# Kernel optimization log

Measured on AMD Instinct MI355X. Metric: run time of the kernel, lower is better.

Reference implementation:

```python
import jax, jax.numpy as jnp
import numpy as np
from jax import lax

T, B, E, U, V = 512, 256, 512, 1024, 50257
H1, H2, L = 512, 256, 2


def setup_inputs() -> dict:
    key = jax.random.key(0)
    ks = jax.random.split(key, 12)
    s = lambda n: 1.0 / np.sqrt(n)
    return {
        "inputs": jax.random.randint(ks[0], (T, B), 0, V, dtype=jnp.int32),
        "input_lengths": jax.random.randint(ks[1], (B,), 1, T + 1, dtype=jnp.int32),
        "embedder": jax.random.normal(ks[2], (V, E), jnp.float32),
        # GRU params (TF GRUCell layout: gates over [x, h] -> 2U; candidate over [x, r*h] -> U)
        "W_gates": jax.random.normal(ks[3], (E + U, 2 * U), jnp.float32) * s(E + U),
        "b_gates": jnp.ones((2 * U,), jnp.float32),  # TF bias init 1.0
        "W_cand": jax.random.normal(ks[4], (E + U, U), jnp.float32) * s(E + U),
        "b_cand": jnp.zeros((U,), jnp.float32),
        # MLP (fully_connected default activation = relu; final layer linear)
        "W1": jax.random.normal(ks[5], (U, H1), jnp.float32) * s(U),
        "b1": jnp.zeros((H1,), jnp.float32),
        "W2": jax.random.normal(ks[6], (H1, H2), jnp.float32) * s(H1),
        "b2": jnp.zeros((H2,), jnp.float32),
        "W3": jax.random.normal(ks[7], (H2, L), jnp.float32) * s(H2),
        "b3": jnp.zeros((L,), jnp.float32),
    }


def reference(inputs, input_lengths, embedder, W_gates, b_gates, W_cand, b_cand,
              W1, b1, W2, b2, W3, b3):
    emb = embedder[inputs]  # [T, B, E] (time-major, as in batch_embedding_lookup)
    t_idx = jnp.arange(emb.shape[0], dtype=input_lengths.dtype)

    def step(h, xt):
        x, t = xt
        xh = jnp.concatenate([x, h], axis=-1)                      # [B, E+U]
        r, z = jnp.split(jax.nn.sigmoid(xh @ W_gates + b_gates), 2, axis=-1)
        cand = jnp.tanh(jnp.concatenate([x, r * h], axis=-1) @ W_cand + b_cand)
        h_new = z * h + (1.0 - z) * cand                           # TF GRUCell update
        # dynamic_rnn sequence_length semantics: state held past end of sequence
        h_out = jnp.where((t < input_lengths)[:, None], h_new, h)
        return h_out, None

    h0 = jnp.zeros((emb.shape[1], U), emb.dtype)
    h_final, _ = lax.scan(step, h0, (emb, t_idx))                  # [B, U]

    x = jax.nn.relu(h_final @ W1 + b1)
    x = jax.nn.relu(x @ W2 + b2)
    logits = x @ W3 + b3                                           # [B, 2]
    predictions = jax.nn.softmax(logits, axis=-1)
    return logits, predictions
```

## Files before the change

kernel.cpp:

```cpp
#include <hip/hip_runtime.h>

typedef unsigned short u16;
typedef unsigned int u32;
typedef unsigned long long u64;

using bf16x8 = __attribute__((ext_vector_type(8))) __bf16;
using f32x4  = __attribute__((ext_vector_type(4))) float;

#define T_DIM 512
#define B_DIM 256
#define E_DIM 512
#define U_DIM 1024
#define K_DIM 1536
#define NG    2048
#define NWG   256

__device__ __forceinline__ u16 f2bf(float f) {
  union { float f; u32 u; } v; v.f = f;
  return (u16)((v.u + 0x7fffu + ((v.u >> 16) & 1u)) >> 16);
}

#define WAIT_VM_ALL() do { asm volatile("s_waitcnt vmcnt(0)" ::: "memory"); \
                           __builtin_amdgcn_sched_barrier(0); } while (0)

#define LD16T(dst, base, OFS) \
  asm volatile("global_load_dwordx4 %0, %1, off offset:" #OFS " sc0 sc1" \
               : "=&v"(dst) : "v"(base))

#define LOAD32T(arr, b) do { \
  const u16* _b0 = (b);           const u16* _b1 = (b) + 2048;  \
  const u16* _b2 = (b) + 4096;    const u16* _b3 = (b) + 6144;  \
  const u16* _b4 = (b) + 8192;    const u16* _b5 = (b) + 10240; \
  const u16* _b6 = (b) + 12288;   const u16* _b7 = (b) + 14336; \
  LD16T(arr[0],  _b0, 0); LD16T(arr[1],  _b0, 1024); \
  LD16T(arr[2],  _b0, 2048); LD16T(arr[3],  _b0, 3072); \
  LD16T(arr[4],  _b1, 0); LD16T(arr[5],  _b1, 1024); \
  LD16T(arr[6],  _b1, 2048); LD16T(arr[7],  _b1, 3072); \
  LD16T(arr[8],  _b2, 0); LD16T(arr[9],  _b2, 1024); \
  LD16T(arr[10], _b2, 2048); LD16T(arr[11], _b2, 3072); \
  LD16T(arr[12], _b3, 0); LD16T(arr[13], _b3, 1024); \
  LD16T(arr[14], _b3, 2048); LD16T(arr[15], _b3, 3072); \
  LD16T(arr[16], _b4, 0); LD16T(arr[17], _b4, 1024); \
  LD16T(arr[18], _b4, 2048); LD16T(arr[19], _b4, 3072); \
  LD16T(arr[20], _b5, 0); LD16T(arr[21], _b5, 1024); \
  LD16T(arr[22], _b5, 2048); LD16T(arr[23], _b5, 3072); \
  LD16T(arr[24], _b6, 0); LD16T(arr[25], _b6, 1024); \
  LD16T(arr[26], _b6, 2048); LD16T(arr[27], _b6, 3072); \
  LD16T(arr[28], _b7, 0); LD16T(arr[29], _b7, 1024); \
  LD16T(arr[30], _b7, 2048); LD16T(arr[31], _b7, 3072); \
} while (0)

__device__ __forceinline__ void st_u64_coh(u64* p, u64 v) {
  u64 r = __hip_atomic_exchange(p, v, __ATOMIC_RELAXED,
                                __HIP_MEMORY_SCOPE_AGENT);
  asm volatile("" :: "v"(r));
}

__global__ __launch_bounds__(256) void init_kernel(float* hF, u16* hB, int* bar) {
  int i = blockIdx.x * 256 + threadIdx.x;
  hF[i] = 0.f;
  hB[i] = 0;
  if (i < 8192) bar[i] = 0;
}

__global__ __launch_bounds__(256) void wconv_kernel(const float* __restrict__ W,
                                                    u16* __restrict__ Wt, int N) {
  int k = blockIdx.x * 64 + (threadIdx.x & 63);
  int n = blockIdx.y * 4 + (threadIdx.x >> 6);
  Wt[(size_t)n * K_DIM + k] = f2bf(W[(size_t)k * N + n]);
}

__global__ __launch_bounds__(128) void embed_kernel(const int* __restrict__ inp,
                                                    const float* __restrict__ emb,
                                                    u16* __restrict__ X) {
  int rb = blockIdx.x;
  int idx = inp[rb];
  int e = threadIdx.x * 4;
  float4 v = *(const float4*)&emb[(size_t)idx * E_DIM + e];
  ushort4 o;
  o.x = f2bf(v.x); o.y = f2bf(v.y); o.z = f2bf(v.z); o.w = f2bf(v.w);
  *(ushort4*)&X[(size_t)rb * E_DIM + e] = o;
}

__device__ __forceinline__ bf16x8 ldsW(const u16* Wl, int lc, int k) {
  int ofs = lc * 3072 + k * 2;
  ofs ^= ((lc & 7) << 4);
  return *(const bf16x8*)((const char*)Wl + ofs);
}

__device__ __forceinline__ void wave_arrive(int* fbase, int ct, int wv,
                                            int phase, int lane) {
  WAIT_VM_ALL();
  if (lane == 0) {
    int r = __hip_atomic_exchange(&fbase[(ct * 4 + wv) * 8], phase,
                                  __ATOMIC_RELAXED, __HIP_MEMORY_SCOPE_AGENT);
    asm volatile("" :: "v"(r));
  }
}
__device__ __forceinline__ int barrier_wait(int* fbase, int phase,
                                            int* sh_tok) {
  int v;
  do {
    v = __hip_atomic_load(&fbase[threadIdx.x * 8], __ATOMIC_RELAXED,
                          __HIP_MEMORY_SCOPE_AGENT);
    if (v >= phase) break;
    __builtin_amdgcn_s_sleep(1);
  } while (true);
  if (threadIdx.x == 0) *sh_tok = (v >> 30);
  __syncthreads();
  return *sh_tok;
}

__global__ void __launch_bounds__(256, 1) gru_loop(
    const u16* __restrict__ X, const u16* __restrict__ WgT,
    const u16* __restrict__ WcT, const float* __restrict__ bg,
    const float* __restrict__ bc, float* __restrict__ hF,
    u16* __restrict__ hB, u16* __restrict__ rhB,
    const int* __restrict__ lens, int* bar) {
  __shared__ __align__(16) u16 Wl[48 * K_DIM];
  __shared__ int sh_tok;
  const int tid = threadIdx.x;
  const int wgid = blockIdx.x;
  const int ct = wgid >> 2;
  const int mq = wgid & 3;

#pragma unroll 4
  for (int it = 0; it < 36; ++it) {
    int ci = it * 256 + tid;
    int lc = ci / 192;
    int k0 = (ci - lc * 192) * 8;
    const u16* src = (lc < 16)
        ? WgT + (size_t)(ct * 16 + lc) * K_DIM + k0
        : (lc < 32)
          ? WgT + (size_t)(1024 + ct * 16 + (lc - 16)) * K_DIM + k0
          : WcT + (size_t)(ct * 16 + (lc - 32)) * K_DIM + k0;
    uint4 v = *(const uint4*)src;
    int ofs = lc * 3072 + k0 * 2;
    ofs ^= ((lc & 7) << 4);
    *(uint4*)((char*)Wl + ofs) = v;
  }
  __syncthreads();

  const int lane = tid & 63, wv = tid >> 6;
  const int l15 = lane & 15;
  const int kq8 = (lane >> 4) * 8;
  const int lq4 = (lane >> 4) * 4;
  const int rbase = mq * 64 + wv * 16;
  const int tbase = (rbase >> 4) * 16384 + (lane >> 4) * 128 + l15 * 8;
  const u16* Hp = hB + tbase;
  const u16* Rp = rhB + tbase;
  int* fbase = bar + mq * 2048;

  int len4[4];
#pragma unroll
  for (int q = 0; q < 4; ++q) len4[q] = lens[rbase + lq4 + q];
  const int nc = ct * 16 + l15;
  const float bg0 = bg[nc];
  const float bg1 = bg[1024 + nc];
  const float bc0 = bc[nc];
  u16* rhW = rhB + (rbase >> 4) * 16384 + (nc >> 3) * 128 + (nc & 7);
  u16* hW  = hB  + (rbase >> 4) * 16384 + (nc >> 3) * 128 + (nc & 7);

  float h_reg[4] = {0.f, 0.f, 0.f, 0.f};
  float z_reg[4];

  bf16x8 af[16], ah[32];
  f32x4 a0 = {0.f, 0.f, 0.f, 0.f};
  {
    const u16* Xt = X + ((size_t)0 * B_DIM + rbase + l15) * E_DIM + kq8;
#pragma unroll
    for (int kb = 0; kb < 16; ++kb) af[kb] = *(const bf16x8*)(Xt + kb * 32);
    WAIT_VM_ALL();
#pragma unroll
    for (int kb = 0; kb < 16; ++kb) {
      a0 = __builtin_amdgcn_mfma_f32_16x16x32_bf16(af[kb],
              ldsW(Wl, l15, kb * 32 + kq8), a0, 0, 0, 0);
    }
  }

  int phase = 0;
  int tok = 0;
  for (int t = 0; t < T_DIM; ++t) {
    const u16* HpT = Hp + tok;
    LOAD32T(ah, HpT);
    WAIT_VM_ALL();
#pragma unroll
    for (int kb = 0; kb < 32; ++kb) {
      a0 = __builtin_amdgcn_mfma_f32_16x16x32_bf16(ah[kb],
              ldsW(Wl, l15, (kb + 16) * 32 + kq8), a0, 0, 0, 0);
    }
#pragma unroll
    for (int q = 0; q < 4; ++q) {
      float r = 1.f / (1.f + __expf(-(a0[q] + bg0)));
      u16 rv = f2bf(r * h_reg[q]);
      u32 lo = (u32)rv | ((u32)(u16)__shfl_xor((int)rv, 1) << 16);
      u32 hi = (u32)__shfl_xor((int)lo, 2);
      if ((l15 & 3) == 0) {
        st_u64_coh((u64*)(rhW + (lq4 + q) * 8), (u64)lo | ((u64)hi << 32));
      }
    }
    wave_arrive(fbase, ct, wv, ++phase, lane);
    f32x4 a1 = {0.f, 0.f, 0.f, 0.f};
#pragma unroll
    for (int kb = 0; kb < 16; ++kb) {
      a1 = __builtin_amdgcn_mfma_f32_16x16x32_bf16(af[kb],
              ldsW(Wl, 16 + l15, kb * 32 + kq8), a1, 0, 0, 0);
    }
#pragma unroll
    for (int kb = 0; kb < 32; ++kb) {
      a1 = __builtin_amdgcn_mfma_f32_16x16x32_bf16(ah[kb],
              ldsW(Wl, 16 + l15, (kb + 16) * 32 + kq8), a1, 0, 0, 0);
    }
#pragma unroll
    for (int q = 0; q < 4; ++q)
      z_reg[q] = 1.f / (1.f + __expf(-(a1[q] + bg1)));
    f32x4 a2 = {0.f, 0.f, 0.f, 0.f};
#pragma unroll
    for (int kb = 0; kb < 16; ++kb) {
      a2 = __builtin_amdgcn_mfma_f32_16x16x32_bf16(af[kb],
              ldsW(Wl, 32 + l15, kb * 32 + kq8), a2, 0, 0, 0);
    }
    tok = barrier_wait(fbase, phase, &sh_tok);

    const u16* RpT = Rp + tok;
    LOAD32T(ah, RpT);
    WAIT_VM_ALL();
#pragma unroll
    for (int kb = 0; kb < 32; ++kb) {
      a2 = __builtin_amdgcn_mfma_f32_16x16x32_bf16(ah[kb],
              ldsW(Wl, 32 + l15, (kb + 16) * 32 + kq8), a2, 0, 0, 0);
    }
#pragma unroll
    for (int q = 0; q < 4; ++q) {
      int row = rbase + lq4 + q;
      float c = tanhf(a2[q] + bc0);
      float hn = z_reg[q] * h_reg[q] + (1.f - z_reg[q]) * c;
      float v = (t < len4[q]) ? hn : h_reg[q];
      h_reg[q] = v;
      u16 hv = f2bf(v);
      u32 lo = (u32)hv | ((u32)(u16)__shfl_xor((int)hv, 1) << 16);
      u32 hi = (u32)__shfl_xor((int)lo, 2);
      if ((l15 & 3) == 0) {
        st_u64_coh((u64*)(hW + (lq4 + q) * 8), (u64)lo | ((u64)hi << 32));
      }
      if (t == T_DIM - 1) {
        hF[(size_t)row * U_DIM + nc] = v;
      }
    }
    wave_arrive(fbase, ct, wv, ++phase, lane);
    a0 = f32x4{0.f, 0.f, 0.f, 0.f};
    if (t + 1 < T_DIM) {
      const u16* Xt = X + ((size_t)(t + 1) * B_DIM + rbase + l15) * E_DIM + kq8;
#pragma unroll
      for (int kb = 0; kb < 16; ++kb) af[kb] = *(const bf16x8*)(Xt + kb * 32);
      WAIT_VM_ALL();
#pragma unroll
      for (int kb = 0; kb < 16; ++kb) {
        a0 = __builtin_amdgcn_mfma_f32_16x16x32_bf16(af[kb],
                ldsW(Wl, l15, kb * 32 + kq8), a0, 0, 0, 0);
      }
    }
    tok = barrier_wait(fbase, phase, &sh_tok);
  }
}

__global__ __launch_bounds__(256) void mlp1_kernel(const float* __restrict__ h,
                                                   const float* __restrict__ W1,
                                                   const float* __restrict__ b1,
                                                   float* __restrict__ o1) {
  int m = blockIdx.x, tid = threadIdx.x;
  __shared__ float xs[1024];
  for (int k = tid; k < 1024; k += 256) xs[k] = h[(size_t)m * 1024 + k];
  __syncthreads();
  for (int n = tid; n < 512; n += 256) {
    float s = b1[n];
    for (int k = 0; k < 1024; ++k) s += xs[k] * W1[(size_t)k * 512 + n];
    o1[(size_t)m * 512 + n] = fmaxf(s, 0.f);
  }
}

__global__ __launch_bounds__(256) void mlp2_kernel(const float* __restrict__ x,
                                                   const float* __restrict__ W2,
                                                   const float* __restrict__ b2,
                                                   float* __restrict__ o2) {
  int m = blockIdx.x, tid = threadIdx.x;
  __shared__ float xs[512];
  for (int k = tid; k < 512; k += 256) xs[k] = x[(size_t)m * 512 + k];
  __syncthreads();
  int n = tid;
  float s = b2[n];
  for (int k = 0; k < 512; ++k) s += xs[k] * W2[(size_t)k * 256 + n];
  o2[(size_t)m * 256 + n] = fmaxf(s, 0.f);
}

__global__ __launch_bounds__(256) void mlp3_kernel(const float* __restrict__ x,
                                                   const float* __restrict__ W3,
                                                   const float* __restrict__ b3,
                                                   float* __restrict__ out) {
  int m = blockIdx.x, tid = threadIdx.x;
  float xk = x[(size_t)m * 256 + tid];
  float p0 = xk * W3[tid * 2 + 0];
  float p1 = xk * W3[tid * 2 + 1];
#pragma unroll
  for (int off = 32; off; off >>= 1) {
    p0 += __shfl_down(p0, off);
    p1 += __shfl_down(p1, off);
  }
  __shared__ float s0[4], s1[4];
  int wave = tid >> 6, lane = tid & 63;
  if (lane == 0) { s0[wave] = p0; s1[wave] = p1; }
  __syncthreads();
  if (tid == 0) {
    float l0 = s0[0] + s0[1] + s0[2] + s0[3] + b3[0];
    float l1 = s1[0] + s1[1] + s1[2] + s1[3] + b3[1];
    out[m * 2 + 0] = l0;
    out[m * 2 + 1] = l1;
    float mx = fmaxf(l0, l1);
    float e0 = __expf(l0 - mx), e1 = __expf(l1 - mx);
    float inv = 1.f / (e0 + e1);
    out[512 + m * 2 + 0] = e0 * inv;
    out[512 + m * 2 + 1] = e1 * inv;
  }
}

extern "C" void kernel_launch(void* const* d_in, const int* in_sizes, int n_in,
                              void* d_out, int out_size, void* d_ws, size_t ws_size,
                              hipStream_t stream) {
  (void)in_sizes; (void)n_in; (void)out_size; (void)ws_size;
  const int* inputs = (const int*)d_in[0];
  const int* lens = (const int*)d_in[1];
  const float* embedder = (const float*)d_in[2];
  const float* Wg = (const float*)d_in[3];
  const float* bg = (const float*)d_in[4];
  const float* Wc = (const float*)d_in[5];
  const float* bc = (const float*)d_in[6];
  const float* W1 = (const float*)d_in[7];
  const float* b1 = (const float*)d_in[8];
  const float* W2 = (const float*)d_in[9];
  const float* b2 = (const float*)d_in[10];
  const float* W3 = (const float*)d_in[11];
  const float* b3 = (const float*)d_in[12];
  float* out = (float*)d_out;

  char* ws = (char*)d_ws;
  size_t off = 0;
  u16* X = (u16*)(ws + off);       off += (size_t)T_DIM * B_DIM * E_DIM * 2;
  u16* WgT = (u16*)(ws + off);     off += (size_t)NG * K_DIM * 2;
  u16* WcT = (u16*)(ws + off);     off += (size_t)U_DIM * K_DIM * 2;
  float* hF = (float*)(ws + off);  off += (size_t)B_DIM * U_DIM * 4;
  u16* hB = (u16*)(ws + off);      off += (size_t)B_DIM * U_DIM * 2;
  u16* rhB = (u16*)(ws + off);     off += (size_t)B_DIM * U_DIM * 2;
  float* o1 = (float*)(ws + off);  off += (size_t)B_DIM * 512 * 4;
  float* o2 = (float*)(ws + off);  off += (size_t)B_DIM * 256 * 4;
  int* bar = (int*)(ws + off);     off += 65536;

  init_kernel<<<dim3(1024), dim3(256), 0, stream>>>(hF, hB, bar);
  wconv_kernel<<<dim3(24, 512), dim3(256), 0, stream>>>(Wg, WgT, NG);
  wconv_kernel<<<dim3(24, 256), dim3(256), 0, stream>>>(Wc, WcT, U_DIM);
  embed_kernel<<<dim3(T_DIM * B_DIM), dim3(128), 0, stream>>>(inputs, embedder, X);

  gru_loop<<<dim3(NWG), dim3(256), 0, stream>>>(X, WgT, WcT, bg, bc, hF, hB, rhB,
                                                lens, bar);

  mlp1_kernel<<<dim3(256), dim3(256), 0, stream>>>(hF, W1, b1, o1);
  mlp2_kernel<<<dim3(256), dim3(256), 0, stream>>>(o1, W2, b2, o2);
  mlp3_kernel<<<dim3(256), dim3(256), 0, stream>>>(o2, W3, b3, out);
}
```

Measured before the change: 7.050 ms.

## Use 512-thread workgroups with per-wave batch-domain barriers in GRU loop

The persistent GRU kernel now runs 128 workgroups of 512 threads instead of 256 of 256. Each workgroup covers a 16-column slice for half the batch, so each weight tile is loaded into LDS once per 8 waves rather than once per 4. The block-wide barrier with __syncthreads is replaced by per-wave flag waits: each 16-row batch slice gets its own flag domain, so a wave only waits on the 64 waves sharing its rows. This removes intra-workgroup syncs and shrinks the barrier scope, at the cost of more waves per CU and higher register pressure.

```diff
diff --git a/kernel.cpp b/kernel.cpp
--- a/kernel.cpp
+++ b/kernel.cpp
@@ -13,7 +13,7 @@
 #define U_DIM 1024
 #define K_DIM 1536
 #define NG    2048
-#define NWG   256
+#define NWG   128
 
 __device__ __forceinline__ u16 f2bf(float f) {
   union { float f; u32 u; } v; v.f = f;
@@ -60,7 +60,7 @@
   int i = blockIdx.x * 256 + threadIdx.x;
   hF[i] = 0.f;
   hB[i] = 0;
-  if (i < 8192) bar[i] = 0;
+  if (i < 16384) bar[i] = 0;
 }
 
 __global__ __launch_bounds__(256) void wconv_kernel(const float* __restrict__ W,
@@ -88,45 +88,41 @@
   return *(const bf16x8*)((const char*)Wl + ofs);
 }
 
-__device__ __forceinline__ void wave_arrive(int* fbase, int ct, int wv,
-                                            int phase, int lane) {
+__device__ __forceinline__ void wave_arrive(int* fdom, int ct, int phase,
+                                            int lane) {
   WAIT_VM_ALL();
   if (lane == 0) {
-    int r = __hip_atomic_exchange(&fbase[(ct * 4 + wv) * 8], phase,
-                                  __ATOMIC_RELAXED, __HIP_MEMORY_SCOPE_AGENT);
+    int r = __hip_atomic_exchange(&fdom[ct * 8], phase, __ATOMIC_RELAXED,
+                                  __HIP_MEMORY_SCOPE_AGENT);
     asm volatile("" :: "v"(r));
   }
 }
-__device__ __forceinline__ int barrier_wait(int* fbase, int phase,
-                                            int* sh_tok) {
+__device__ __forceinline__ int wave_wait(int* fdom, int phase, int lane) {
   int v;
   do {
-    v = __hip_atomic_load(&fbase[threadIdx.x * 8], __ATOMIC_RELAXED,
+    v = __hip_atomic_load(&fdom[(lane & 63) * 8], __ATOMIC_RELAXED,
                           __HIP_MEMORY_SCOPE_AGENT);
     if (v >= phase) break;
     __builtin_amdgcn_s_sleep(1);
   } while (true);
-  if (threadIdx.x == 0) *sh_tok = (v >> 30);
-  __syncthreads();
-  return *sh_tok;
-}
-
-__global__ void __launch_bounds__(256, 1) gru_loop(
+  return v >> 30;
+}
+
+__global__ void __launch_bounds__(512, 2) gru_loop(
     const u16* __restrict__ X, const u16* __restrict__ WgT,
     const u16* __restrict__ WcT, const float* __restrict__ bg,
     const float* __restrict__ bc, float* __restrict__ hF,
     u16* __restrict__ hB, u16* __restrict__ rhB,
     const int* __restrict__ lens, int* bar) {
   __shared__ __align__(16) u16 Wl[48 * K_DIM];
-  __shared__ int sh_tok;
   const int tid = threadIdx.x;
   const int wgid = blockIdx.x;
-  const int ct = wgid >> 2;
-  const int mq = wgid & 3;
+  const int ct = wgid >> 1;
+  const int half = wgid & 1;
 
 #pragma unroll 4
-  for (int it = 0; it < 36; ++it) {
-    int ci = it * 256 + tid;
+  for (int it = 0; it < 18; ++it) {
+    int ci = it * 512 + tid;
     int lc = ci / 192;
     int k0 = (ci - lc * 192) * 8;
     const u16* src = (lc < 16)
@@ -145,11 +141,12 @@
   const int l15 = lane & 15;
   const int kq8 = (lane >> 4) * 8;
   const int lq4 = (lane >> 4) * 4;
-  const int rbase = mq * 64 + wv * 16;
+  const int d = half * 8 + wv;
+  const int rbase = d * 16;
   const int tbase = (rbase >> 4) * 16384 + (lane >> 4) * 128 + l15 * 8;
   const u16* Hp = hB + tbase;
   const u16* Rp = rhB + tbase;
-  int* fbase = bar + mq * 2048;
+  int* fdom = bar + d * 1024;
 
   int len4[4];
 #pragma unroll
@@ -199,7 +196,7 @@
         st_u64_coh((u64*)(rhW + (lq4 + q) * 8), (u64)lo | ((u64)hi << 32));
       }
     }
-    wave_arrive(fbase, ct, wv, ++phase, lane);
+    wave_arrive(fdom, ct, ++phase, lane);
     f32x4 a1 = {0.f, 0.f, 0.f, 0.f};
 #pragma unroll
     for (int kb = 0; kb < 16; ++kb) {
@@ -220,7 +217,7 @@
       a2 = __builtin_amdgcn_mfma_f32_16x16x32_bf16(af[kb],
               ldsW(Wl, 32 + l15, kb * 32 + kq8), a2, 0, 0, 0);
     }
-    tok = barrier_wait(fbase, phase, &sh_tok);
+    tok = wave_wait(fdom, phase, lane);
 
     const u16* RpT = Rp + tok;
     LOAD32T(ah, RpT);
@@ -247,7 +244,7 @@
         hF[(size_t)row * U_DIM + nc] = v;
       }
     }
-    wave_arrive(fbase, ct, wv, ++phase, lane);
+    wave_arrive(fdom, ct, ++phase, lane);
     a0 = f32x4{0.f, 0.f, 0.f, 0.f};
     if (t + 1 < T_DIM) {
       const u16* Xt = X + ((size_t)(t + 1) * B_DIM + rbase + l15) * E_DIM + kq8;
@@ -260,7 +257,7 @@
                 ldsW(Wl, l15, kb * 32 + kq8), a0, 0, 0, 0);
       }
     }
-    tok = barrier_wait(fbase, phase, &sh_tok);
+    tok = wave_wait(fdom, phase, lane);
   }
 }
 
@@ -359,7 +356,7 @@
   wconv_kernel<<<dim3(24, 256), dim3(256), 0, stream>>>(Wc, WcT, U_DIM);
   embed_kernel<<<dim3(T_DIM * B_DIM), dim3(128), 0, stream>>>(inputs, embedder, X);
 
-  gru_loop<<<dim3(NWG), dim3(256), 0, stream>>>(X, WgT, WcT, bg, bc, hF, hB, rhB,
+  gru_loop<<<dim3(NWG), dim3(512), 0, stream>>>(X, WgT, WcT, bg, bc, hF, hB, rhB,
                                                 lens, bar);
 
   mlp1_kernel<<<dim3(256), dim3(256), 0, stream>>>(hF, W1, b1, o1);
```

Result: slower. 23.17 ms (+228.6%).
